# Performance work log

Measured on AMD Instinct MI355X. Metric: run time of the kernel, lower is better.

Reference implementation:

```python
import jax, jax.numpy as jnp
import numpy as np

N_HEADS = 32
N_KV_HEADS = 8
HEAD_DIM = 128
N_REP = N_HEADS // N_KV_HEADS


def apply_rope(x, cos, sin):
    # x: [B, S, H, D]; cos/sin: [S_max, D//2]
    S = x.shape[1]
    c = cos[:S][None, :, None, :]
    s = sin[:S][None, :, None, :]
    x_even = x[..., ::2]
    x_odd = x[..., 1::2]
    out = jnp.stack([x_even * c - x_odd * s, x_even * s + x_odd * c], axis=-1)
    return out.reshape(x.shape)


def setup_inputs() -> dict:
    key = jax.random.key(0)
    ks = jax.random.split(key, 8)
    B, S, D = 2, 2048, 4096
    x = jax.random.normal(ks[0], (B, S, D), dtype=jnp.float32)
    # RoPE tables
    pos = jnp.arange(S, dtype=jnp.float32)[:, None]
    inv_freq = 1.0 / (10000.0 ** (jnp.arange(0, HEAD_DIM, 2, dtype=jnp.float32) / HEAD_DIM))
    ang = pos * inv_freq[None, :]  # [S, HEAD_DIM//2]
    cos = jnp.cos(ang)
    sin = jnp.sin(ang)
    # causal additive mask [1,1,S,S]
    tril = jnp.tril(jnp.ones((S, S), dtype=bool))
    mask = jnp.where(tril, 0.0, -1e9).astype(jnp.float32)[None, None]
    sc = 0.02
    Wq = jax.random.normal(ks[1], (D, N_HEADS * HEAD_DIM), dtype=jnp.float32) * sc
    Wk = jax.random.normal(ks[2], (D, N_KV_HEADS * HEAD_DIM), dtype=jnp.float32) * sc
    Wv = jax.random.normal(ks[3], (D, N_KV_HEADS * HEAD_DIM), dtype=jnp.float32) * sc
    Wo = jax.random.normal(ks[4], (N_HEADS * HEAD_DIM, D), dtype=jnp.float32) * sc
    return {"x": x, "cos": cos, "sin": sin, "mask": mask,
            "Wq": Wq, "Wk": Wk, "Wv": Wv, "Wo": Wo}


def reference(x, cos, sin, mask, Wq, Wk, Wv, Wo):
    B, S, D = x.shape
    q = (x @ Wq).reshape(B, S, N_HEADS, HEAD_DIM)
    k = (x @ Wk).reshape(B, S, N_KV_HEADS, HEAD_DIM)
    v = (x @ Wv).reshape(B, S, N_KV_HEADS, HEAD_DIM)
    q = apply_rope(q, cos, sin)
    k = apply_rope(k, cos, sin)
    # repeat_interleave KV heads to match query heads
    k = jnp.repeat(k, N_REP, axis=2)
    v = jnp.repeat(v, N_REP, axis=2)
    q = q.transpose(0, 2, 1, 3)  # [B, H, S, D]
    k = k.transpose(0, 2, 1, 3)
    v = v.transpose(0, 2, 1, 3)
    scale = HEAD_DIM ** -0.5
    scores = jnp.einsum('bhqd,bhkd->bhqk', q, k) * scale + mask
    attn = jax.nn.softmax(scores, axis=-1)
    out = jnp.einsum('bhqk,bhkd->bhqd', attn, v)
    out = out.transpose(0, 2, 1, 3).reshape(B, S, N_HEADS * HEAD_DIM)
    return out @ Wo
```

## Files before the change

### kernel.cpp

```cpp
#include <hip/hip_runtime.h>

typedef __attribute__((ext_vector_type(8))) short short8;
typedef __attribute__((ext_vector_type(4))) float f32x4;
typedef __attribute__((ext_vector_type(16))) float f32x16;
typedef __attribute__((ext_vector_type(4))) unsigned short u16x4;
typedef __attribute__((ext_vector_type(8))) unsigned short u16x8;

typedef __attribute__((address_space(3))) void lds_void;
typedef __attribute__((address_space(1))) void g_void;

#define GL16(g, l) __builtin_amdgcn_global_load_lds((g_void*)(g), (lds_void*)(l), 16, 0, 0)
#define EXP2F(x) __builtin_exp2f(x)

__device__ inline float b2f(unsigned short u) {
  union { unsigned u; float f; } v; v.u = ((unsigned)u) << 16; return v.f;
}
__device__ inline unsigned short f2b(float f) {
  union { float f; unsigned u; } v; v.f = f;
  unsigned r = v.u + 0x7FFFu + ((v.u >> 16) & 1u);
  return (unsigned short)(r >> 16);
}
__device__ inline unsigned short f2b_rne(float f) {
  unsigned u;
  asm("v_cvt_pk_bf16_f32 %0, %1, %2" : "=v"(u) : "v"(f), "v"(f));
  return (unsigned short)u;
}
__device__ inline unsigned short cvtb(float v) { return f2b(v); }
__device__ inline unsigned short cvtb(unsigned short v) { return v; }

__global__ __launch_bounds__(256) void conv_f32_bf16(const float* __restrict__ in,
                                                     unsigned short* __restrict__ out, long n) {
  long i = ((long)blockIdx.x * 256 + threadIdx.x) * 4;
  if (i >= n) return;
  f32x4 v = *(const f32x4*)(in + i);
  u16x4 o;
  o[0] = f2b(v[0]); o[1] = f2b(v[1]); o[2] = f2b(v[2]); o[3] = f2b(v[3]);
  *(u16x4*)(out + i) = o;
}

template <typename TIN>
__global__ __launch_bounds__(256) void transpose_bf16(const TIN* __restrict__ in,
                                                      unsigned short* __restrict__ out,
                                                      int R, int C, int ldin) {
  __shared__ unsigned short tile[32][33];
  int c0 = blockIdx.x * 32, r0 = blockIdx.y * 32;
  int tx = threadIdx.x & 31, ty = threadIdx.x >> 5;
#pragma unroll
  for (int i = ty; i < 32; i += 8)
    tile[i][tx] = cvtb(in[(long)(r0 + i) * ldin + c0 + tx]);
  __syncthreads();
#pragma unroll
  for (int i = ty; i < 32; i += 8)
    out[(long)(c0 + i) * R + r0 + tx] = tile[tx][i];
}

template <int MODE>
__global__ __launch_bounds__(256, 3) void gemm_m97(const unsigned short* __restrict__ A,
                                                   const unsigned short* __restrict__ Bt,
                                                   void* __restrict__ C,
                                                   const float* __restrict__ cosp,
                                                   const float* __restrict__ sinp,
                                                   int M, int N, int K) {
  __shared__ unsigned short As[128 * 64];
  __shared__ unsigned short Bs[128 * 64];
  const int tid = threadIdx.x;
  const int lane = tid & 63;
  const int wid = tid >> 6;
  const int wr = wid >> 1, wc = wid & 1;
  const int l31 = lane & 31, lh = lane >> 5;
  const int xr = l31 & 7;
  const int nbn = N >> 7;
  const int bm = blockIdx.x / nbn, bn = blockIdx.x % nbn;

  const long K2 = (long)K * 2;
  const int csw = ((tid & 7) ^ ((tid >> 3) & 7)) << 4;
  const char* gA = (const char*)A + ((long)bm * 128 + (tid >> 3)) * K2 + csw;
  const char* gB = (const char*)Bt + ((long)bn * 128 + (tid >> 3)) * K2 + csw;
  char* dA = (char*)As + tid * 16;
  char* dB = (char*)Bs + tid * 16;

  f32x16 acc[2][2];
#pragma unroll
  for (int m = 0; m < 2; m++)
#pragma unroll
    for (int n = 0; n < 2; n++)
#pragma unroll
      for (int i = 0; i < 16; i++) acc[m][n][i] = 0.f;

  const int offA0 = (wr * 64 + l31) * 128;
  const int offB0 = (wc * 64 + l31) * 128;

  const int NT = K >> 6;
  for (int t = 0; t < NT; ++t) {
    __syncthreads();
    const long ko = (long)t * 128;
    GL16(gA + ko, dA);
    GL16(gA + ko + 32 * K2, dA + 4096);
    GL16(gA + ko + 64 * K2, dA + 8192);
    GL16(gA + ko + 96 * K2, dA + 12288);
    GL16(gB + ko, dB);
    GL16(gB + ko + 32 * K2, dB + 4096);
    GL16(gB + ko + 64 * K2, dB + 8192);
    GL16(gB + ko + 96 * K2, dB + 12288);
    __syncthreads();
#pragma unroll
    for (int kk = 0; kk < 4; kk++) {
      const int co = (((kk * 2 + lh) ^ xr) << 4);
      short8 a0 = *(const short8*)((const char*)As + offA0 + co);
      short8 a1 = *(const short8*)((const char*)As + offA0 + 4096 + co);
      short8 b0 = *(const short8*)((const char*)Bs + offB0 + co);
      short8 b1 = *(const short8*)((const char*)Bs + offB0 + 4096 + co);
      acc[0][0] = __builtin_amdgcn_mfma_f32_32x32x16_bf16(a0, b0, acc[0][0], 0, 0, 0);
      acc[0][1] = __builtin_amdgcn_mfma_f32_32x32x16_bf16(a0, b1, acc[0][1], 0, 0, 0);
      acc[1][0] = __builtin_amdgcn_mfma_f32_32x32x16_bf16(a1, b0, acc[1][0], 0, 0, 0);
      acc[1][1] = __builtin_amdgcn_mfma_f32_32x32x16_bf16(a1, b1, acc[1][1], 0, 0, 0);
    }
  }

  const long crow0 = (long)bm * 128 + wr * 64 + 4 * lh;
  const int ccol0 = bn * 128 + wc * 64 + l31;
  const float qscale = 0.08838834764831845f * 1.44269504088896341f;
#pragma unroll
  for (int m = 0; m < 2; m++)
#pragma unroll
    for (int n = 0; n < 2; n++)
#pragma unroll
      for (int reg = 0; reg < 16; reg++) {
        long row = crow0 + m * 32 + (reg & 3) + 8 * (reg >> 2);
        int col = ccol0 + n * 32;
        float v = acc[m][n][reg];
        if (MODE == 0) {
          ((float*)C)[row * N + col] = v;
        } else {
          float other = __shfl_xor(v, 1, 64);
          float out = v;
          if (col < 5120) {
            int s = (int)(row & 2047);
            int ib = (col & 127) >> 1;
            float cc = cosp[s * 64 + ib], ss = sinp[s * 64 + ib];
            out = (col & 1) ? (other * ss + v * cc) : (v * cc - other * ss);
            if (col < 4096) out *= qscale;
          }
          ((unsigned short*)C)[row * N + col] = f2b_rne(out);
        }
      }
}

__global__ __launch_bounds__(256) void attn_kernel(const unsigned short* __restrict__ QKV,
                                                   const unsigned short* __restrict__ Vt,
                                                   unsigned short* __restrict__ O,
                                                   int S, int BS) {
  __shared__ unsigned short Ks[64 * 128];
  __shared__ unsigned short Vs[128 * 64];
  __shared__ unsigned short Ps[4][16 * 68];
  const int tid = threadIdx.x, wave = tid >> 6, lane = tid & 63;
  const int lrow = lane & 15, kgrp = lane >> 4;
  const int nqt = S >> 6, nqt2 = nqt >> 1;
  int bid = blockIdx.x;
  const int qp = bid % nqt2; bid /= nqt2;
  const int h = bid & 31;
  const int b = bid >> 5;
  const int kh = h >> 2;
  const long rowbase = (long)b * S;

  const char* kg = (const char*)(QKV + rowbase * 6144 + 4096 + kh * 128)
                   + (tid >> 4) * 12288 + (((tid & 15) ^ ((tid >> 4) & 7)) * 16);
  const char* vg = (const char*)(Vt + (long)(kh * 128 + (tid >> 3)) * BS + rowbase)
                   + (((tid & 7) ^ ((tid >> 3) & 7)) * 16);
  char* lK = (char*)Ks + wave * 1024;
  char* lV = (char*)Vs + wave * 1024;

  for (int pass = 0; pass < 2; pass++) {
    const int qt = pass ? (nqt - 1 - qp) : qp;
    const int qbase = qt * 64;
    const int q0 = qbase + wave * 16;

    short8 qf[4];
    {
      const unsigned short* qpt = QKV + (rowbase + q0 + lrow) * 6144 + h * 128 + kgrp * 8;
#pragma unroll
      for (int dc = 0; dc < 4; dc++) qf[dc] = *(const short8*)(qpt + dc * 32);
    }
    f32x4 oacc[8];
#pragma unroll
    for (int dt = 0; dt < 8; dt++) oacc[dt] = (f32x4){0.f, 0.f, 0.f, 0.f};
    float mrun[4] = {-1e30f, -1e30f, -1e30f, -1e30f};
    float lrun[4] = {0.f, 0.f, 0.f, 0.f};

    const int kv_end = qbase + 64;
    for (int kv0 = 0; kv0 < kv_end; kv0 += 64) {
      __syncthreads();
#pragma unroll
      for (int p = 0; p < 4; p++)
        GL16(kg + (long)(kv0 + p * 16) * 12288, lK + p * 4096);
#pragma unroll
      for (int p = 0; p < 4; p++)
        GL16(vg + (long)kv0 * 2 + (long)p * 32 * BS * 2, lV + p * 4096);
      __syncthreads();

      f32x4 sc[4];
#pragma unroll
      for (int n = 0; n < 4; n++) {
        f32x4 s = (f32x4){0.f, 0.f, 0.f, 0.f};
#pragma unroll
        for (int dc = 0; dc < 4; dc++) {
          short8 kf = *(const short8*)(Ks + (n * 16 + lrow) * 128 + (((dc * 4 + kgrp) ^ (lrow & 7)) << 3));
          s = __builtin_amdgcn_mfma_f32_16x16x32_bf16(qf[dc], kf, s, 0, 0, 0);
        }
        sc[n] = s;
      }

      if (kv0 + 63 > q0) {
#pragma unroll
        for (int r = 0; r < 4; r++) {
          const int qg = q0 + kgrp * 4 + r;
#pragma unroll
          for (int n = 0; n < 4; n++) {
            int kgi = kv0 + n * 16 + lrow;
            if (kgi > qg) sc[n][r] = -1e30f;
          }
        }
      }

      float mx[4];
#pragma unroll
      for (int r = 0; r < 4; r++) {
        float m0 = fmaxf(fmaxf(sc[0][r], sc[1][r]), fmaxf(sc[2][r], sc[3][r]));
#pragma unroll
        for (int d = 1; d < 16; d <<= 1) m0 = fmaxf(m0, __shfl_xor(m0, d, 64));
        mx[r] = m0;
      }
      bool grow = false;
#pragma unroll
      for (int r = 0; r < 4; r++) grow = grow || (mx[r] > mrun[r] + 8.f);

      if (__all(!grow)) {
#pragma unroll
        for (int r = 0; r < 4; r++) {
          float psum = 0.f;
#pragma unroll
          for (int n = 0; n < 4; n++) {
            float pv = EXP2F(sc[n][r] - mrun[r]);
            psum += pv;
            Ps[wave][(kgrp * 4 + r) * 68 + n * 16 + lrow] = f2b_rne(pv);
          }
          lrun[r] += psum;
        }
      } else {
#pragma unroll
        for (int r = 0; r < 4; r++) {
          float mnew = fmaxf(mrun[r], mx[r]);
          float corr = EXP2F(mrun[r] - mnew);
          mrun[r] = mnew;
          float psum = 0.f;
#pragma unroll
          for (int n = 0; n < 4; n++) {
            float pv = EXP2F(sc[n][r] - mnew);
            psum += pv;
            Ps[wave][(kgrp * 4 + r) * 68 + n * 16 + lrow] = f2b_rne(pv);
          }
          lrun[r] = lrun[r] * corr + psum;
#pragma unroll
          for (int dt = 0; dt < 8; dt++) oacc[dt][r] *= corr;
        }
      }
      asm volatile("s_waitcnt lgkmcnt(0)" ::: "memory");
#pragma unroll
      for (int kc = 0; kc < 2; kc++) {
        short8 pa = *(const short8*)(&Ps[wave][lrow * 68 + kc * 32 + kgrp * 8]);
#pragma unroll
        for (int dt = 0; dt < 8; dt++) {
          short8 vb = *(const short8*)(Vs + (dt * 16 + lrow) * 64 + (((kc * 4 + kgrp) ^ (lrow & 7)) << 3));
          oacc[dt] = __builtin_amdgcn_mfma_f32_16x16x32_bf16(pa, vb, oacc[dt], 0, 0, 0);
        }
      }
    }

    float inv[4];
#pragma unroll
    for (int r = 0; r < 4; r++) {
      float l = lrun[r];
#pragma unroll
      for (int d = 1; d < 16; d <<= 1) l += __shfl_xor(l, d, 64);
      inv[r] = 1.f / l;
    }
    unsigned short* op = O + (rowbase + q0 + kgrp * 4) * 4096 + h * 128 + lrow;
#pragma unroll
    for (int dt = 0; dt < 8; dt++)
#pragma unroll
      for (int r = 0; r < 4; r++)
        op[(long)r * 4096 + dt * 16] = f2b_rne(oacc[dt][r] * inv[r]);
  }
}

extern "C" void kernel_launch(void* const* d_in, const int* in_sizes, int n_in,
                              void* d_out, int out_size, void* d_ws, size_t ws_size,
                              hipStream_t stream) {
  const float* x = (const float*)d_in[0];
  const float* cosp = (const float*)d_in[1];
  const float* sinp = (const float*)d_in[2];
  const float* Wq = (const float*)d_in[4];
  const float* Wk = (const float*)d_in[5];
  const float* Wv = (const float*)d_in[6];
  const float* Wo = (const float*)d_in[7];
  const int S = 2048;
  const long M = 4096;

  if (ws_size < 176160768ULL) return;

  char* ws = (char*)d_ws;
  unsigned short* xb   = (unsigned short*)(ws);
  unsigned short* Wqt  = (unsigned short*)(ws + 33554432);
  unsigned short* Wkt  = (unsigned short*)(ws + 67108864);
  unsigned short* Wvt  = (unsigned short*)(ws + 75497472);
  unsigned short* Wot  = (unsigned short*)(ws + 83886080);
  unsigned short* QKVb = (unsigned short*)(ws + 117440512);
  unsigned short* Vtg  = (unsigned short*)(ws + 167772160);
  unsigned short* AO   = xb;

  conv_f32_bf16<<<16384, 256, 0, stream>>>(x, xb, M * 4096);
  transpose_bf16<float><<<dim3(128, 128), 256, 0, stream>>>(Wq, Wqt, 4096, 4096, 4096);
  transpose_bf16<float><<<dim3(32, 128), 256, 0, stream>>>(Wk, Wkt, 4096, 1024, 1024);
  transpose_bf16<float><<<dim3(32, 128), 256, 0, stream>>>(Wv, Wvt, 4096, 1024, 1024);
  transpose_bf16<float><<<dim3(128, 128), 256, 0, stream>>>(Wo, Wot, 4096, 4096, 4096);

  gemm_m97<2><<<1536, 256, 0, stream>>>(xb, Wqt, QKVb, cosp, sinp, 4096, 6144, 4096);
  transpose_bf16<unsigned short><<<dim3(32, 128), 256, 0, stream>>>(QKVb + 5120, Vtg, 4096, 1024, 6144);

  attn_kernel<<<1024, 256, 0, stream>>>(QKVb, Vtg, AO, S, 4096);

  gemm_m97<0><<<1024, 256, 0, stream>>>(AO, Wot, d_out, nullptr, nullptr, 4096, 4096, 4096);
}
```

Baseline: 659.4 us.

## Process two 64-row query tiles per attention block to share KV loads; merge weight prep

Each attention block now handles 128 query rows as two 64-row halves that share every K/V tile staged in shared memory. This roughly halves global K/V traffic and barrier count per query row, and the block count drops from 1024 to 512. The cost is doubled accumulator registers, which may lower occupancy. The four weight transpose launches are merged into one kernel, and the output GEMM's launch bounds minimum-blocks hint rises from 3 to 4.

```diff
diff --git a/kernel.cpp b/kernel.cpp
--- a/kernel.cpp
+++ b/kernel.cpp
@@ -25,8 +25,6 @@
   asm("v_cvt_pk_bf16_f32 %0, %1, %2" : "=v"(u) : "v"(f), "v"(f));
   return (unsigned short)u;
 }
-__device__ inline unsigned short cvtb(float v) { return f2b(v); }
-__device__ inline unsigned short cvtb(unsigned short v) { return v; }
 
 __global__ __launch_bounds__(256) void conv_f32_bf16(const float* __restrict__ in,
                                                      unsigned short* __restrict__ out, long n) {
@@ -38,29 +36,53 @@
   *(u16x4*)(out + i) = o;
 }
 
-template <typename TIN>
-__global__ __launch_bounds__(256) void transpose_bf16(const TIN* __restrict__ in,
-                                                      unsigned short* __restrict__ out,
-                                                      int R, int C, int ldin) {
+__global__ __launch_bounds__(256) void prep_weights(const float* __restrict__ Wq,
+                                                    const float* __restrict__ Wk,
+                                                    const float* __restrict__ Wv,
+                                                    const float* __restrict__ Wo,
+                                                    unsigned short* __restrict__ Wqkv,
+                                                    unsigned short* __restrict__ Wot) {
+  __shared__ unsigned short tile[32][33];
+  int id = blockIdx.x;
+  const float* src; unsigned short* dst; int C;
+  if (id < 16384)      { src = Wq; dst = Wqkv;            C = 4096; }
+  else if (id < 20480) { src = Wk; dst = Wqkv + 16777216; C = 1024; id -= 16384; }
+  else if (id < 24576) { src = Wv; dst = Wqkv + 20971520; C = 1024; id -= 20480; }
+  else                 { src = Wo; dst = Wot;             C = 4096; id -= 24576; }
+  const int nbx = C >> 5;
+  const int c0 = (id % nbx) * 32, r0 = (id / nbx) * 32;
+  const int tx = threadIdx.x & 31, ty = threadIdx.x >> 5;
+#pragma unroll
+  for (int i = ty; i < 32; i += 8)
+    tile[i][tx] = f2b(src[(long)(r0 + i) * C + c0 + tx]);
+  __syncthreads();
+#pragma unroll
+  for (int i = ty; i < 32; i += 8)
+    dst[(long)(c0 + i) * 4096 + r0 + tx] = tile[tx][i];
+}
+
+__global__ __launch_bounds__(256) void transpose_u16(const unsigned short* __restrict__ in,
+                                                     unsigned short* __restrict__ out,
+                                                     int R, int C, int ldin) {
   __shared__ unsigned short tile[32][33];
   int c0 = blockIdx.x * 32, r0 = blockIdx.y * 32;
   int tx = threadIdx.x & 31, ty = threadIdx.x >> 5;
 #pragma unroll
   for (int i = ty; i < 32; i += 8)
-    tile[i][tx] = cvtb(in[(long)(r0 + i) * ldin + c0 + tx]);
+    tile[i][tx] = in[(long)(r0 + i) * ldin + c0 + tx];
   __syncthreads();
 #pragma unroll
   for (int i = ty; i < 32; i += 8)
     out[(long)(c0 + i) * R + r0 + tx] = tile[tx][i];
 }
 
-template <int MODE>
-__global__ __launch_bounds__(256, 3) void gemm_m97(const unsigned short* __restrict__ A,
-                                                   const unsigned short* __restrict__ Bt,
-                                                   void* __restrict__ C,
-                                                   const float* __restrict__ cosp,
-                                                   const float* __restrict__ sinp,
-                                                   int M, int N, int K) {
+template <int MODE, int MINB>
+__global__ __launch_bounds__(256, MINB) void gemm_m97(const unsigned short* __restrict__ A,
+                                                      const unsigned short* __restrict__ Bt,
+                                                      void* __restrict__ C,
+                                                      const float* __restrict__ cosp,
+                                                      const float* __restrict__ sinp,
+                                                      int M, int N, int K) {
   __shared__ unsigned short As[128 * 64];
   __shared__ unsigned short Bs[128 * 64];
   const int tid = threadIdx.x;
@@ -155,9 +177,9 @@
   __shared__ unsigned short Ps[4][16 * 68];
   const int tid = threadIdx.x, wave = tid >> 6, lane = tid & 63;
   const int lrow = lane & 15, kgrp = lane >> 4;
-  const int nqt = S >> 6, nqt2 = nqt >> 1;
+  const int nqt = S >> 7, nqp = nqt >> 1;
   int bid = blockIdx.x;
-  const int qp = bid % nqt2; bid /= nqt2;
+  const int qp = bid % nqp; bid /= nqp;
   const int h = bid & 31;
   const int b = bid >> 5;
   const int kh = h >> 2;
@@ -172,23 +194,28 @@
 
   for (int pass = 0; pass < 2; pass++) {
     const int qt = pass ? (nqt - 1 - qp) : qp;
-    const int qbase = qt * 64;
-    const int q0 = qbase + wave * 16;
-
-    short8 qf[4];
-    {
-      const unsigned short* qpt = QKV + (rowbase + q0 + lrow) * 6144 + h * 128 + kgrp * 8;
-#pragma unroll
-      for (int dc = 0; dc < 4; dc++) qf[dc] = *(const short8*)(qpt + dc * 32);
-    }
-    f32x4 oacc[8];
-#pragma unroll
-    for (int dt = 0; dt < 8; dt++) oacc[dt] = (f32x4){0.f, 0.f, 0.f, 0.f};
-    float mrun[4] = {-1e30f, -1e30f, -1e30f, -1e30f};
-    float lrun[4] = {0.f, 0.f, 0.f, 0.f};
-
-    const int kv_end = qbase + 64;
-    for (int kv0 = 0; kv0 < kv_end; kv0 += 64) {
+    const int qbase = qt * 128;
+
+    short8 qf[2][4];
+#pragma unroll
+    for (int u = 0; u < 2; u++) {
+      const unsigned short* qpt =
+          QKV + (rowbase + qbase + u * 64 + wave * 16 + lrow) * 6144 + h * 128 + kgrp * 8;
+#pragma unroll
+      for (int dc = 0; dc < 4; dc++) qf[u][dc] = *(const short8*)(qpt + dc * 32);
+    }
+    f32x4 oacc[2][8];
+    float mrun[2][4], lrun[2][4];
+#pragma unroll
+    for (int u = 0; u < 2; u++) {
+#pragma unroll
+      for (int dt = 0; dt < 8; dt++) oacc[u][dt] = (f32x4){0.f, 0.f, 0.f, 0.f};
+#pragma unroll
+      for (int r = 0; r < 4; r++) { mrun[u][r] = -1e30f; lrun[u][r] = 0.f; }
+    }
+
+    const int kv_end1 = qbase + 128;
+    for (int kv0 = 0; kv0 < kv_end1; kv0 += 64) {
       __syncthreads();
 #pragma unroll
       for (int p = 0; p < 4; p++)
@@ -198,98 +225,107 @@
         GL16(vg + (long)kv0 * 2 + (long)p * 32 * BS * 2, lV + p * 4096);
       __syncthreads();
 
-      f32x4 sc[4];
-#pragma unroll
-      for (int n = 0; n < 4; n++) {
-        f32x4 s = (f32x4){0.f, 0.f, 0.f, 0.f};
-#pragma unroll
-        for (int dc = 0; dc < 4; dc++) {
-          short8 kf = *(const short8*)(Ks + (n * 16 + lrow) * 128 + (((dc * 4 + kgrp) ^ (lrow & 7)) << 3));
-          s = __builtin_amdgcn_mfma_f32_16x16x32_bf16(qf[dc], kf, s, 0, 0, 0);
-        }
-        sc[n] = s;
+#pragma unroll
+      for (int u = 0; u < 2; u++) {
+        if (kv0 >= qbase + 64 + u * 64) continue;
+        const int q0 = qbase + u * 64 + wave * 16;
+
+        f32x4 sc[4];
+#pragma unroll
+        for (int n = 0; n < 4; n++) {
+          f32x4 s = (f32x4){0.f, 0.f, 0.f, 0.f};
+#pragma unroll
+          for (int dc = 0; dc < 4; dc++) {
+            short8 kf = *(const short8*)(Ks + (n * 16 + lrow) * 128 + (((dc * 4 + kgrp) ^ (lrow & 7)) << 3));
+            s = __builtin_amdgcn_mfma_f32_16x16x32_bf16(qf[u][dc], kf, s, 0, 0, 0);
+          }
+          sc[n] = s;
+        }
+
+        if (kv0 + 63 > q0) {
+#pragma unroll
+          for (int r = 0; r < 4; r++) {
+            const int qg = q0 + kgrp * 4 + r;
+#pragma unroll
+            for (int n = 0; n < 4; n++) {
+              int kgi = kv0 + n * 16 + lrow;
+              if (kgi > qg) sc[n][r] = -1e30f;
+            }
+          }
+        }
+
+        float mx[4];
+#pragma unroll
+        for (int r = 0; r < 4; r++) {
+          float m0 = fmaxf(fmaxf(sc[0][r], sc[1][r]), fmaxf(sc[2][r], sc[3][r]));
+#pragma unroll
+          for (int d = 1; d < 16; d <<= 1) m0 = fmaxf(m0, __shfl_xor(m0, d, 64));
+          mx[r] = m0;
+        }
+        bool grow = false;
+#pragma unroll
+        for (int r = 0; r < 4; r++) grow = grow || (mx[r] > mrun[u][r] + 8.f);
+
+        if (__all(!grow)) {
+#pragma unroll
+          for (int r = 0; r < 4; r++) {
+            float psum = 0.f;
+#pragma unroll
+            for (int n = 0; n < 4; n++) {
+              float pv = EXP2F(sc[n][r] - mrun[u][r]);
+              psum += pv;
+              Ps[wave][(kgrp * 4 + r) * 68 + n * 16 + lrow] = f2b_rne(pv);
+            }
+            lrun[u][r] += psum;
+          }
+        } else {
+#pragma unroll
+          for (int r = 0; r < 4; r++) {
+            float mnew = fmaxf(mrun[u][r], mx[r]);
+            float corr = EXP2F(mrun[u][r] - mnew);
+            mrun[u][r] = mnew;
+            float psum = 0.f;
+#pragma unroll
+            for (int n = 0; n < 4; n++) {
+              float pv = EXP2F(sc[n][r] - mnew);
+              psum += pv;
+              Ps[wave][(kgrp * 4 + r) * 68 + n * 16 + lrow] = f2b_rne(pv);
+            }
+            lrun[u][r] = lrun[u][r] * corr + psum;
+#pragma unroll
+            for (int dt = 0; dt < 8; dt++) oacc[u][dt][r] *= corr;
+          }
+        }
+        asm volatile("s_waitcnt lgkmcnt(0)" ::: "memory");
+#pragma unroll
+        for (int kc = 0; kc < 2; kc++) {
+          short8 pa = *(const short8*)(&Ps[wave][lrow * 68 + kc * 32 + kgrp * 8]);
+#pragma unroll
+          for (int dt = 0; dt < 8; dt++) {
+            short8 vb = *(const short8*)(Vs + (dt * 16 + lrow) * 64 + (((kc * 4 + kgrp) ^ (lrow & 7)) << 3));
+            oacc[u][dt] = __builtin_amdgcn_mfma_f32_16x16x32_bf16(pa, vb, oacc[u][dt], 0, 0, 0);
+          }
+        }
       }
-
-      if (kv0 + 63 > q0) {
-#pragma unroll
-        for (int r = 0; r < 4; r++) {
-          const int qg = q0 + kgrp * 4 + r;
-#pragma unroll
-          for (int n = 0; n < 4; n++) {
-            int kgi = kv0 + n * 16 + lrow;
-            if (kgi > qg) sc[n][r] = -1e30f;
-          }
-        }
+    }
+
+#pragma unroll
+    for (int u = 0; u < 2; u++) {
+      float inv[4];
+#pragma unroll
+      for (int r = 0; r < 4; r++) {
+        float l = lrun[u][r];
+#pragma unroll
+        for (int d = 1; d < 16; d <<= 1) l += __shfl_xor(l, d, 64);
+        inv[r] = 1.f / l;
       }
-
-      float mx[4];
-#pragma unroll
-      for (int r = 0; r < 4; r++) {
-        float m0 = fmaxf(fmaxf(sc[0][r], sc[1][r]), fmaxf(sc[2][r], sc[3][r]));
-#pragma unroll
-        for (int d = 1; d < 16; d <<= 1) m0 = fmaxf(m0, __shfl_xor(m0, d, 64));
-        mx[r] = m0;
-      }
-      bool grow = false;
-#pragma unroll
-      for (int r = 0; r < 4; r++) grow = grow || (mx[r] > mrun[r] + 8.f);
-
-      if (__all(!grow)) {
-#pragma unroll
-        for (int r = 0; r < 4; r++) {
-          float psum = 0.f;
-#pragma unroll
-          for (int n = 0; n < 4; n++) {
-            float pv = EXP2F(sc[n][r] - mrun[r]);
-            psum += pv;
-            Ps[wave][(kgrp * 4 + r) * 68 + n * 16 + lrow] = f2b_rne(pv);
-          }
-          lrun[r] += psum;
-        }
-      } else {
-#pragma unroll
-        for (int r = 0; r < 4; r++) {
-          float mnew = fmaxf(mrun[r], mx[r]);
-          float corr = EXP2F(mrun[r] - mnew);
-          mrun[r] = mnew;
-          float psum = 0.f;
-#pragma unroll
-          for (int n = 0; n < 4; n++) {
-            float pv = EXP2F(sc[n][r] - mnew);
-            psum += pv;
-            Ps[wave][(kgrp * 4 + r) * 68 + n * 16 + lrow] = f2b_rne(pv);
-          }
-          lrun[r] = lrun[r] * corr + psum;
-#pragma unroll
-          for (int dt = 0; dt < 8; dt++) oacc[dt][r] *= corr;
-        }
-      }
-      asm volatile("s_waitcnt lgkmcnt(0)" ::: "memory");
-#pragma unroll
-      for (int kc = 0; kc < 2; kc++) {
-        short8 pa = *(const short8*)(&Ps[wave][lrow * 68 + kc * 32 + kgrp * 8]);
-#pragma unroll
-        for (int dt = 0; dt < 8; dt++) {
-          short8 vb = *(const short8*)(Vs + (dt * 16 + lrow) * 64 + (((kc * 4 + kgrp) ^ (lrow & 7)) << 3));
-          oacc[dt] = __builtin_amdgcn_mfma_f32_16x16x32_bf16(pa, vb, oacc[dt], 0, 0, 0);
-        }
-      }
-    }
-
-    float inv[4];
-#pragma unroll
-    for (int r = 0; r < 4; r++) {
-      float l = lrun[r];
-#pragma unroll
-      for (int d = 1; d < 16; d <<= 1) l += __shfl_xor(l, d, 64);
-      inv[r] = 1.f / l;
-    }
-    unsigned short* op = O + (rowbase + q0 + kgrp * 4) * 4096 + h * 128 + lrow;
-#pragma unroll
-    for (int dt = 0; dt < 8; dt++)
-#pragma unroll
-      for (int r = 0; r < 4; r++)
-        op[(long)r * 4096 + dt * 16] = f2b_rne(oacc[dt][r] * inv[r]);
+      unsigned short* op = O + (rowbase + qbase + u * 64 + wave * 16 + kgrp * 4) * 4096 + h * 128 + lrow;
+#pragma unroll
+      for (int dt = 0; dt < 8; dt++)
+#pragma unroll
+        for (int r = 0; r < 4; r++)
+          op[(long)r * 4096 + dt * 16] = f2b_rne(oacc[u][dt][r] * inv[r]);
+    }
   }
 }
 
@@ -311,23 +347,18 @@
   char* ws = (char*)d_ws;
   unsigned short* xb   = (unsigned short*)(ws);
   unsigned short* Wqt  = (unsigned short*)(ws + 33554432);
-  unsigned short* Wkt  = (unsigned short*)(ws + 67108864);
-  unsigned short* Wvt  = (unsigned short*)(ws + 75497472);
   unsigned short* Wot  = (unsigned short*)(ws + 83886080);
   unsigned short* QKVb = (unsigned short*)(ws + 117440512);
   unsigned short* Vtg  = (unsigned short*)(ws + 167772160);
   unsigned short* AO   = xb;
 
   conv_f32_bf16<<<16384, 256, 0, stream>>>(x, xb, M * 4096);
-  transpose_bf16<float><<<dim3(128, 128), 256, 0, stream>>>(Wq, Wqt, 4096, 4096, 4096);
-  transpose_bf16<float><<<dim3(32, 128), 256, 0, stream>>>(Wk, Wkt, 4096, 1024, 1024);
-  transpose_bf16<float><<<dim3(32, 128), 256, 0, stream>>>(Wv, Wvt, 4096, 1024, 1024);
-  transpose_bf16<float><<<dim3(128, 128), 256, 0, stream>>>(Wo, Wot, 4096, 4096, 4096);
-
-  gemm_m97<2><<<1536, 256, 0, stream>>>(xb, Wqt, QKVb, cosp, sinp, 4096, 6144, 4096);
-  transpose_bf16<unsigned short><<<dim3(32, 128), 256, 0, stream>>>(QKVb + 5120, Vtg, 4096, 1024, 6144);
-
-  attn_kernel<<<1024, 256, 0, stream>>>(QKVb, Vtg, AO, S, 4096);
-
-  gemm_m97<0><<<1024, 256, 0, stream>>>(AO, Wot, d_out, nullptr, nullptr, 4096, 4096, 4096);
-}
+  prep_weights<<<40960, 256, 0, stream>>>(Wq, Wk, Wv, Wo, Wqt, Wot);
+
+  gemm_m97<2, 3><<<1536, 256, 0, stream>>>(xb, Wqt, QKVb, cosp, sinp, 4096, 6144, 4096);
+  transpose_u16<<<dim3(32, 128), 256, 0, stream>>>(QKVb + 5120, Vtg, 4096, 1024, 6144);
+
+  attn_kernel<<<512, 256, 0, stream>>>(QKVb, Vtg, AO, S, 4096);
+
+  gemm_m97<0, 4><<<1024, 256, 0, stream>>>(AO, Wot, d_out, nullptr, nullptr, 4096, 4096, 4096);
+}
```

After: 731.1 us. 10.9% more time.
